# Kernel tuning notes

Measured on AMD Instinct MI355X. Metric: run time of the kernel, lower is better.

## Reference

```python
import jax, jax.numpy as jnp
import numpy as np

B, T, DIM, H = 32, 1024, 512, 8
HD = DIM // H
HID = int(DIM * 4.0)
EPS = 1e-6
SCALE = HD ** -0.5


def _ln(t, g, b):
    m = t.mean(-1, keepdims=True)
    var = ((t - m) ** 2).mean(-1, keepdims=True)
    return (t - m) * jax.lax.rsqrt(var + EPS) * g + b


def setup_inputs() -> dict:
    key = jax.random.key(0)
    ks = jax.random.split(key, 10)
    n = lambda k, s: jax.random.normal(k, s, dtype=jnp.float32)
    w = lambda k, s: n(k, s) * 0.02
    z = lambda d: jnp.zeros((d,), dtype=jnp.float32)
    o = lambda d: jnp.ones((d,), dtype=jnp.float32)
    return {
        'x': n(ks[0], (B, T, DIM)),
        'k': n(ks[1], (T, H, B, HD)),
        'v': n(ks[2], (T, H, B, HD)),
        'Wqkv': w(ks[3], (DIM, 3 * DIM)), 'bqkv': z(3 * DIM),
        'Wsa': w(ks[4], (DIM, DIM)), 'bsa': z(DIM),
        'Wq': w(ks[5], (DIM, DIM)), 'bq': z(DIM),
        'Wed': w(ks[6], (DIM, DIM)), 'bed': z(DIM),
        'g1': o(DIM), 'be1': z(DIM),
        'g2': o(DIM), 'be2': z(DIM),
        'g3': o(DIM), 'be3': z(DIM),
        'W1': w(ks[7], (DIM, HID)), 'b1': z(HID),
        'W2': w(ks[8], (HID, DIM)), 'b2': z(DIM),
    }


def _decoder_block(x, k, v, Wqkv, bqkv, Wsa, bsa, Wq, bq, Wed, bed,
                   g1, be1, g2, be2, g3, be3, W1, b1, W2, b2):
    # ---- self-attention (faithful to the original, degenerate einsums) ----
    qkv = x @ Wqkv + bqkv                                        # [B,T,3*DIM]
    qkv = qkv.reshape(B, T, 3, H, HD).transpose(2, 1, 3, 0, 4)   # [3,T,H,B,HD]
    q, sk, sv = qkv[0], qkv[1], qkv[2]
    dp = jnp.einsum('kabc,qdef->qabe', sk, q) * SCALE            # [T,H,B,B]
    scores = jax.nn.softmax(dp, axis=-1)
    wa = jnp.einsum('qabc,kdef->bqaf', scores, sv).reshape(B, T, DIM)
    attn = wa @ Wsa + bsa
    an1 = _ln(attn + x, g1, be1)
    # ---- encoder-decoder attention ----
    qe = (an1 @ Wq + bq).reshape(B, T, H, HD).transpose(1, 2, 0, 3)  # [T,H,B,HD]
    dp2 = jnp.einsum('abkd,abqd->abqk', k, qe) * SCALE           # [T,H,B,B]
    sc2 = jax.nn.softmax(dp2, axis=-1)
    wa2 = jnp.einsum('abts,abse->tabe', sc2, v).reshape(B, T, DIM)
    attn2 = wa2 @ Wed + bed
    an2 = _ln(attn2 + x, g2, be2)
    # ---- MLP (exact GELU, as nn.GELU default) ----
    hmid = jax.nn.gelu(an2 @ W1 + b1, approximate=False)
    z = hmid @ W2 + b2
    return _ln(z + an2, g3, be3)


def reference(x, k, v, Wqkv, bqkv, Wsa, bsa, Wq, bq, Wed, bed,
              g1, be1, g2, be2, g3, be3, W1, b1, W2, b2):
    return _decoder_block(x, k, v, Wqkv, bqkv, Wsa, bsa, Wq, bq, Wed, bed,
                          g1, be1, g2, be2, g3, be3, W1, b1, W2, b2)
```

## Files before the change

### kernel.cpp

```cpp
#include <hip/hip_runtime.h>
#include <hip/hip_bf16.h>
#include <math.h>

#define Bn 32
#define Tn 1024
#define DIMn 512
#define Hn 8
#define HDn 64
#define HIDn 2048
#define Mn 32768

using short8 = __attribute__((ext_vector_type(8))) short;
using half8  = __attribute__((ext_vector_type(8))) _Float16;
using f32x4  = __attribute__((ext_vector_type(4))) float;
typedef unsigned short u16;
typedef unsigned int   u32;

__device__ __forceinline__ u16 f2h(float x) {
  _Float16 h = (_Float16)x;
  return __builtin_bit_cast(u16, h);
}
__device__ __forceinline__ float h2f(u16 u) {
  return (float)__builtin_bit_cast(_Float16, u);
}
__device__ __forceinline__ u32 pack2h(float a, float b) {
  return (u32)f2h(a) | ((u32)f2h(b) << 16);
}
__device__ __forceinline__ void gld16(const void* g, void* l) {
  __builtin_amdgcn_global_load_lds((const __attribute__((address_space(1))) u32*)g,
                                   (__attribute__((address_space(3))) u32*)l, 16, 0, 0);
}
__device__ __forceinline__ float wredsum(float v) {
  #pragma unroll
  for (int d = 1; d < 64; d <<= 1) v += __shfl_xor(v, d, 64);
  return v;
}
__device__ __forceinline__ void hard_barrier() {
  asm volatile("" ::: "memory");
  __builtin_amdgcn_s_barrier();
  asm volatile("" ::: "memory");
}
__device__ __forceinline__ float fast_gelu(float v) {
  const float ax = fabsf(v) * 0.70710678118654752f;
  const float t = 1.0f / (1.0f + 0.3275911f * ax);
  const float p = ((((1.061405429f * t - 1.453152027f) * t) + 1.421413741f) * t - 0.284496736f) * t + 0.254829592f;
  const float y = 1.0f - p * t * __expf(-ax * ax);
  const float erfv = (v >= 0.f) ? y : -y;
  return 0.5f * v * (1.0f + erfv);
}

__global__ __launch_bounds__(256) void colsum1(const float* __restrict__ x, float* __restrict__ part) {
  const int b = blockIdx.x, t = threadIdx.x;
  const float* p = x + (size_t)b * 128 * DIMn;
  float a0 = 0.f, a1 = 0.f;
  for (int r = 0; r < 128; ++r) {
    a0 += p[r * DIMn + t];
    a1 += p[r * DIMn + t + 256];
  }
  part[b * DIMn + t] = a0;
  part[b * DIMn + t + 256] = a1;
}

__global__ __launch_bounds__(256) void colsum2(const float* __restrict__ part, float* __restrict__ xs) {
  const int c = blockIdx.x * 256 + threadIdx.x;
  float a = 0.f;
  for (int b = 0; b < 256; ++b) a += part[b * DIMn + c];
  xs[c] = a;
}

__global__ __launch_bounds__(256) void sv_k(const float* __restrict__ xs, const float* __restrict__ Wqkv,
                                            const float* __restrict__ bqkv, float* __restrict__ SVp) {
  __shared__ float xsh[512];
  __shared__ float red[4][64];
  const int h = blockIdx.x, q = threadIdx.x >> 6, f = threadIdx.x & 63;
  xsh[threadIdx.x] = xs[threadIdx.x];
  xsh[threadIdx.x + 256] = xs[threadIdx.x + 256];
  __syncthreads();
  const int colb = 2 * DIMn + h * HDn + f;
  float acc = 0.f;
  for (int i = q * 128; i < q * 128 + 128; ++i) acc += xsh[i] * Wqkv[(size_t)i * 1536 + colb];
  red[q][f] = acc;
  __syncthreads();
  if (q == 0)
    SVp[h * 64 + f] = red[0][f] + red[1][f] + red[2][f] + red[3][f] + 32768.0f * bqkv[colb];
}

__global__ __launch_bounds__(256) void attnc2_k(const float* __restrict__ SVp, const float* __restrict__ Wsa,
                                                const float* __restrict__ bsa, float* __restrict__ attnc) {
  __shared__ float SVs[64];
  __shared__ float red[4][64];
  const int q = threadIdx.x >> 6, jj = threadIdx.x & 63;
  if (threadIdx.x < 64) {
    float s = 0.f;
    #pragma unroll
    for (int h = 0; h < 8; ++h) s += SVp[h * 64 + threadIdx.x];
    SVs[threadIdx.x] = s;
  }
  __syncthreads();
  const int j = blockIdx.x * 64 + jj;
  float acc = 0.f;
  for (int i = q * 128; i < q * 128 + 128; ++i) acc += SVs[i & 63] * Wsa[(size_t)i * DIMn + j];
  red[q][jj] = acc;
  __syncthreads();
  if (q == 0) attnc[j] = red[0][jj] + red[1][jj] + red[2][jj] + red[3][jj] + bsa[j];
}

__global__ __launch_bounds__(256) void wtrans(const float* __restrict__ W, u16* __restrict__ WT, int K, int N) {
  __shared__ float tile[64][65];
  const int n0 = blockIdx.x * 64, k0 = blockIdx.y * 64;
  const int t = threadIdx.x;
  #pragma unroll
  for (int i = 0; i < 16; ++i) {
    const int fl = i * 256 + t, r = fl >> 6, c = fl & 63;
    tile[r][c] = W[(size_t)(k0 + r) * N + n0 + c];
  }
  __syncthreads();
  #pragma unroll
  for (int i = 0; i < 16; ++i) {
    const int fl = i * 256 + t, r = fl >> 6, c = fl & 63;
    WT[(size_t)(n0 + r) * K + k0 + c] = f2h(tile[c][r]);
  }
}

template <int MODE>
__global__ __launch_bounds__(256) void ln_k(const void* __restrict__ Ap, const void* __restrict__ Bp,
                                            const float* __restrict__ cv, const float* __restrict__ g,
                                            const float* __restrict__ be, void* __restrict__ outp) {
  const int row = blockIdx.x * 4 + (threadIdx.x >> 6);
  const int l = threadIdx.x & 63;
  const size_t base = (size_t)row * DIMn + l * 8;
  float v[8];
  if (MODE == 0 || MODE == 2) {
    const float* a = (const float*)Ap + base;
    float4 x0 = *(const float4*)a;
    float4 x1 = *(const float4*)(a + 4);
    v[0] = x0.x; v[1] = x0.y; v[2] = x0.z; v[3] = x0.w;
    v[4] = x1.x; v[5] = x1.y; v[6] = x1.z; v[7] = x1.w;
  } else {
    short8 s = *(const short8*)((const u16*)Ap + base);
    #pragma unroll
    for (int i = 0; i < 8; ++i) v[i] = h2f((u16)s[i]);
  }
  if (MODE == 0) {
    float4 c0 = *(const float4*)(cv + l * 8);
    float4 c1 = *(const float4*)(cv + l * 8 + 4);
    v[0] += c0.x; v[1] += c0.y; v[2] += c0.z; v[3] += c0.w;
    v[4] += c1.x; v[5] += c1.y; v[6] += c1.z; v[7] += c1.w;
  } else if (MODE == 1) {
    const float* b = (const float*)Bp + base;
    float4 x0 = *(const float4*)b;
    float4 x1 = *(const float4*)(b + 4);
    v[0] += x0.x; v[1] += x0.y; v[2] += x0.z; v[3] += x0.w;
    v[4] += x1.x; v[5] += x1.y; v[6] += x1.z; v[7] += x1.w;
  } else {
    short8 s2 = *(const short8*)((const u16*)Bp + base);
    #pragma unroll
    for (int i = 0; i < 8; ++i) v[i] += h2f((u16)s2[i]);
  }
  float s = 0.f;
  #pragma unroll
  for (int i = 0; i < 8; ++i) s += v[i];
  s = wredsum(s);
  const float mean = s * (1.0f / 512.0f);
  float q = 0.f;
  #pragma unroll
  for (int i = 0; i < 8; ++i) { const float d = v[i] - mean; q += d * d; }
  q = wredsum(q);
  const float rs = rsqrtf(q * (1.0f / 512.0f) + 1e-6f);
  float gg[8], bb[8];
  {
    float4 g0 = *(const float4*)(g + l * 8);
    float4 g1 = *(const float4*)(g + l * 8 + 4);
    float4 b0 = *(const float4*)(be + l * 8);
    float4 b1 = *(const float4*)(be + l * 8 + 4);
    gg[0] = g0.x; gg[1] = g0.y; gg[2] = g0.z; gg[3] = g0.w;
    gg[4] = g1.x; gg[5] = g1.y; gg[6] = g1.z; gg[7] = g1.w;
    bb[0] = b0.x; bb[1] = b0.y; bb[2] = b0.z; bb[3] = b0.w;
    bb[4] = b1.x; bb[5] = b1.y; bb[6] = b1.z; bb[7] = b1.w;
  }
  float y[8];
  #pragma unroll
  for (int i = 0; i < 8; ++i) y[i] = (v[i] - mean) * rs * gg[i] + bb[i];
  if (MODE == 2) {
    float* o = (float*)outp + base;
    *(float4*)o = make_float4(y[0], y[1], y[2], y[3]);
    *(float4*)(o + 4) = make_float4(y[4], y[5], y[6], y[7]);
  } else {
    short8 o;
    #pragma unroll
    for (int i = 0; i < 8; ++i) o[i] = (short)f2h(y[i]);
    *(short8*)((u16*)outp + base) = o;
  }
}

#define CPAD 132
template <bool GELU, bool OBF>
__global__ __launch_bounds__(256) void gemm_bt(const u16* __restrict__ A, const u16* __restrict__ BT,
                                               const float* __restrict__ bias, u16* __restrict__ OB,
                                               float* __restrict__ OF, int Ni, int Ki, int gridX) {
  __shared__ u16 smem[3 * 8192];
  const int tid = threadIdx.x;
  const int l = tid & 63, w = tid >> 6, wr = w >> 1, wc = w & 1;

  int wg = blockIdx.x;
  const int nwg = gridDim.x;
  if ((nwg & 7) == 0) {
    const int q = nwg >> 3;
    wg = (wg & 7) * q + (wg >> 3);
  }
  const int bx = wg % gridX, by = wg / gridX;
  const int m0 = by * 128, n0 = bx * 128;
  const int r16 = l & 15, g4 = l >> 4;

  const u16* ga = A + (size_t)(m0 + (tid >> 2)) * (size_t)Ki + (tid & 3) * 8;
  const u16* gb = BT + (size_t)(n0 + (tid >> 2)) * (size_t)Ki + (tid & 3) * 8;
  const int ldst = tid * 8;

  int aoff[4], boff[4];
  #pragma unroll
  for (int i = 0; i < 4; ++i) {
    aoff[i] = (wr * 64 + i * 16 + r16) * 32 + g4 * 8;
    boff[i] = 4096 + (wc * 64 + i * 16 + r16) * 32 + g4 * 8;
  }
  f32x4 acc[4][4] = {};

  const int nt = Ki >> 5;
  auto STAGE = [&](int t, int b) {
    u16* base = smem + b * 8192;
    const int kk = t * 32;
    gld16(ga + kk, &base[ldst]);
    gld16(ga + kk + (size_t)64 * Ki, &base[ldst + 2048]);
    gld16(gb + kk, &base[4096 + ldst]);
    gld16(gb + kk + (size_t)64 * Ki, &base[4096 + ldst + 2048]);
  };

  STAGE(0, 0);
  STAGE(1, 1);
  int b0 = 0, b1 = 1, b2 = 2;
  for (int t = 0; t < nt; ++t) {
    if (t < nt - 1) asm volatile("s_waitcnt vmcnt(4)" ::: "memory");
    else            asm volatile("s_waitcnt vmcnt(0)" ::: "memory");
    hard_barrier();
    if (t + 2 < nt) STAGE(t + 2, b2);
    const u16* base = smem + b0 * 8192;
    half8 af[4], bf[4];
    #pragma unroll
    for (int i = 0; i < 4; ++i) af[i] = *(const half8*)&base[aoff[i]];
    #pragma unroll
    for (int i = 0; i < 4; ++i) bf[i] = *(const half8*)&base[boff[i]];
    #pragma unroll
    for (int mi = 0; mi < 4; ++mi)
      #pragma unroll
      for (int ni = 0; ni < 4; ++ni)
        acc[mi][ni] = __builtin_amdgcn_mfma_f32_16x16x32_f16(af[mi], bf[ni], acc[mi][ni], 0, 0, 0);
    hard_barrier();
    const int tb = b0; b0 = b1; b1 = b2; b2 = tb;
  }

  if (OBF) {
    u16* Cs = smem;
    #pragma unroll
    for (int ni = 0; ni < 4; ++ni) {
      const int col = wc * 64 + ni * 16 + r16;
      const float bv = bias[n0 + col];
      #pragma unroll
      for (int mi = 0; mi < 4; ++mi) {
        const int rowb = wr * 64 + mi * 16 + g4 * 4;
        #pragma unroll
        for (int r = 0; r < 4; ++r) {
          float v = acc[mi][ni][r] + bv;
          if (GELU) v = fast_gelu(v);
          Cs[(rowb + r) * CPAD + col] = f2h(v);
        }
      }
    }
    hard_barrier();
    const int rr = tid >> 4;
    const int c0 = (tid & 15) * 8;
    #pragma unroll
    for (int j = 0; j < 8; ++j) {
      const int row = rr + j * 16;
      *(short8*)(OB + (size_t)(m0 + row) * Ni + n0 + c0) = *(const short8*)&Cs[row * CPAD + c0];
    }
  } else {
    #pragma unroll
    for (int ni = 0; ni < 4; ++ni) {
      const int col = n0 + wc * 64 + ni * 16 + r16;
      const float bv = bias[col];
      #pragma unroll
      for (int mi = 0; mi < 4; ++mi) {
        const int rowb = m0 + wr * 64 + mi * 16 + g4 * 4;
        #pragma unroll
        for (int r = 0; r < 4; ++r) {
          float v = acc[mi][ni][r] + bv;
          if (GELU) v = fast_gelu(v);
          OF[(size_t)(rowb + r) * Ni + col] = v;
        }
      }
    }
  }
}

__global__ __launch_bounds__(64) void attn_k(const u16* __restrict__ qe, const float* __restrict__ kin,
                                             const float* __restrict__ vin, u16* __restrict__ wa2) {
  const int t = blockIdx.x >> 3;
  const int h = blockIdx.x & 7;
  const int l = threadIdx.x;
  __shared__ u16 Kq[32 * 80];
  __shared__ u16 Qq[32 * 80];
  __shared__ u16 VT[64 * 48];
  __shared__ u16 Ps[32 * 48];

  const float* kp = kin + (size_t)blockIdx.x * 2048;
  const float* vp = vin + (size_t)blockIdx.x * 2048;
  #pragma unroll
  for (int i = 0; i < 8; ++i) {
    const int fl = i * 256 + l * 4;
    const int r = fl >> 6, c = fl & 63;
    float4 kv = *(const float4*)(kp + fl);
    float4 vv = *(const float4*)(vp + fl);
    *(u32*)&Kq[r * 80 + c]     = pack2h(kv.x, kv.y);
    *(u32*)&Kq[r * 80 + c + 2] = pack2h(kv.z, kv.w);
    VT[(c + 0) * 48 + r] = f2h(vv.x);
    VT[(c + 1) * 48 + r] = f2h(vv.y);
    VT[(c + 2) * 48 + r] = f2h(vv.z);
    VT[(c + 3) * 48 + r] = f2h(vv.w);
  }
  {
    const int qb = l >> 1, hf = l & 1;
    const u16* qp = qe + (size_t)(qb * Tn + t) * DIMn + h * HDn + hf * 32;
    #pragma unroll
    for (int j = 0; j < 4; ++j) {
      short8 d = *(const short8*)(qp + j * 8);
      *(short8*)&Qq[qb * 80 + hf * 32 + j * 8] = d;
    }
  }
  __syncthreads();

  const int r16 = l & 15, g4 = l >> 4;
  f32x4 sacc[2][2] = {};
  #pragma unroll
  for (int kk = 0; kk < 2; ++kk) {
    half8 aQ0 = *(const half8*)&Qq[r16 * 80 + kk * 32 + g4 * 8];
    half8 aQ1 = *(const half8*)&Qq[(16 + r16) * 80 + kk * 32 + g4 * 8];
    half8 bK0 = *(const half8*)&Kq[r16 * 80 + kk * 32 + g4 * 8];
    half8 bK1 = *(const half8*)&Kq[(16 + r16) * 80 + kk * 32 + g4 * 8];
    sacc[0][0] = __builtin_amdgcn_mfma_f32_16x16x32_f16(aQ0, bK0, sacc[0][0], 0, 0, 0);
    sacc[0][1] = __builtin_amdgcn_mfma_f32_16x16x32_f16(aQ0, bK1, sacc[0][1], 0, 0, 0);
    sacc[1][0] = __builtin_amdgcn_mfma_f32_16x16x32_f16(aQ1, bK0, sacc[1][0], 0, 0, 0);
    sacc[1][1] = __builtin_amdgcn_mfma_f32_16x16x32_f16(aQ1, bK1, sacc[1][1], 0, 0, 0);
  }
  #pragma unroll
  for (int m = 0; m < 2; ++m) {
    #pragma unroll
    for (int r = 0; r < 4; ++r) {
      const float a0 = sacc[m][0][r] * 0.125f;
      const float a1 = sacc[m][1][r] * 0.125f;
      float mx = fmaxf(a0, a1);
      #pragma unroll
      for (int d = 1; d < 16; d <<= 1) mx = fmaxf(mx, __shfl_xor(mx, d, 64));
      const float e0 = __expf(a0 - mx), e1 = __expf(a1 - mx);
      float sm = e0 + e1;
      #pragma unroll
      for (int d = 1; d < 16; d <<= 1) sm += __shfl_xor(sm, d, 64);
      const float inv = 1.0f / sm;
      const int rr = m * 16 + g4 * 4 + r;
      Ps[rr * 48 + r16]      = f2h(e0 * inv);
      Ps[rr * 48 + 16 + r16] = f2h(e1 * inv);
    }
  }
  __syncthreads();

  half8 aP0 = *(const half8*)&Ps[r16 * 48 + g4 * 8];
  half8 aP1 = *(const half8*)&Ps[(16 + r16) * 48 + g4 * 8];
  f32x4 oacc[2][4] = {};
  #pragma unroll
  for (int nn = 0; nn < 4; ++nn) {
    half8 bV = *(const half8*)&VT[(nn * 16 + r16) * 48 + g4 * 8];
    oacc[0][nn] = __builtin_amdgcn_mfma_f32_16x16x32_f16(aP0, bV, oacc[0][nn], 0, 0, 0);
    oacc[1][nn] = __builtin_amdgcn_mfma_f32_16x16x32_f16(aP1, bV, oacc[1][nn], 0, 0, 0);
  }
  #pragma unroll
  for (int m = 0; m < 2; ++m) {
    #pragma unroll
    for (int r = 0; r < 4; ++r) {
      const int qb = m * 16 + g4 * 4 + r;
      u16* op = wa2 + (size_t)(qb * Tn + t) * DIMn + h * HDn;
      #pragma unroll
      for (int nn = 0; nn < 4; ++nn)
        op[nn * 16 + r16] = f2h(oacc[m][nn][r]);
    }
  }
}

extern "C" void kernel_launch(void* const* d_in, const int* in_sizes, int n_in,
                              void* d_out, int out_size, void* d_ws, size_t ws_size,
                              hipStream_t stream) {
  (void)in_sizes; (void)n_in; (void)out_size;
  const float* x    = (const float*)d_in[0];
  const float* kin  = (const float*)d_in[1];
  const float* vin  = (const float*)d_in[2];
  const float* Wqkv = (const float*)d_in[3];
  const float* bqkv = (const float*)d_in[4];
  const float* Wsa  = (const float*)d_in[5];
  const float* bsa  = (const float*)d_in[6];
  const float* Wq   = (const float*)d_in[7];
  const float* bq   = (const float*)d_in[8];
  const float* Wed  = (const float*)d_in[9];
  const float* bed  = (const float*)d_in[10];
  const float* g1   = (const float*)d_in[11];
  const float* be1  = (const float*)d_in[12];
  const float* g2   = (const float*)d_in[13];
  const float* be2  = (const float*)d_in[14];
  const float* g3   = (const float*)d_in[15];
  const float* be3  = (const float*)d_in[16];
  const float* W1   = (const float*)d_in[17];
  const float* b1   = (const float*)d_in[18];
  const float* W2   = (const float*)d_in[19];
  const float* b2   = (const float*)d_in[20];

  char* ws = (char*)d_ws;
  float* xs    = (float*)(ws);
  float* SVp   = (float*)(ws + (2 << 10));
  float* attnc = (float*)(ws + (4 << 10));
  float* part  = (float*)(ws + (6 << 10));
  u16* wqT  = (u16*)(ws + (1 << 20));
  u16* wedT = (u16*)(ws + (1 << 20) + (512 << 10));
  u16* w1T  = (u16*)(ws + (2 << 20));
  u16* w2T  = (u16*)(ws + (4 << 20));
  u16* Abuf = (u16*)(ws + (6 << 20));
  const size_t HOFF = 38ull << 20;
  u16* hmid = (u16*)(ws + HOFF);

  u16* an1  = Abuf;
  u16* wa2  = Abuf;
  u16* an2b = Abuf;
  u16*   qe   = (u16*)d_out;
  u16*   a2bf = (u16*)d_out;
  float* zf   = (float*)d_out;

  long long avail = (long long)ws_size - (long long)HOFF;
  int crows = (avail > 0) ? (int)(avail / (HIDn * 2)) : 128;
  crows = (crows / 128) * 128;
  if (crows < 128) crows = 128;
  if (crows > Mn) crows = Mn;

  colsum1<<<256, 256, 0, stream>>>(x, part);
  colsum2<<<2, 256, 0, stream>>>(part, xs);
  sv_k<<<8, 256, 0, stream>>>(xs, Wqkv, bqkv, SVp);
  attnc2_k<<<8, 256, 0, stream>>>(SVp, Wsa, bsa, attnc);

  wtrans<<<dim3(8, 8),  256, 0, stream>>>(Wq,  wqT,  512, 512);
  wtrans<<<dim3(8, 8),  256, 0, stream>>>(Wed, wedT, 512, 512);
  wtrans<<<dim3(32, 8), 256, 0, stream>>>(W1,  w1T,  512, 2048);
  wtrans<<<dim3(8, 32), 256, 0, stream>>>(W2,  w2T,  2048, 512);

  ln_k<0><<<Mn / 4, 256, 0, stream>>>(x, nullptr, attnc, g1, be1, an1);
  gemm_bt<false, true><<<1024, 256, 0, stream>>>(an1, wqT, bq, qe, nullptr, 512, 512, 4);
  attn_k<<<Tn * Hn, 64, 0, stream>>>(qe, kin, vin, wa2);
  gemm_bt<false, true><<<1024, 256, 0, stream>>>(wa2, wedT, bed, a2bf, nullptr, 512, 512, 4);
  ln_k<1><<<Mn / 4, 256, 0, stream>>>(a2bf, x, nullptr, g2, be2, an2b);
  for (int r0 = 0; r0 < Mn; r0 += crows) {
    int rc = Mn - r0; if (rc > crows) rc = crows;
    gemm_bt<true, true><<<16 * (rc / 128), 256, 0, stream>>>(an2b + (size_t)r0 * DIMn, w1T, b1, hmid, nullptr, HIDn, DIMn, 16);
    gemm_bt<false, false><<<4 * (rc / 128), 256, 0, stream>>>(hmid, w2T, b2, nullptr, zf + (size_t)r0 * DIMn, DIMn, HIDn, 4);
  }
  ln_k<2><<<Mn / 4, 256, 0, stream>>>(zf, an2b, nullptr, g3, be3, d_out);
}
```

Baseline: 428.7 us.

## Enlarge GEMM tiles to 256x256 with 512-thread blocks

```diff
diff --git a/kernel.cpp b/kernel.cpp
--- a/kernel.cpp
+++ b/kernel.cpp
@@ -193,14 +193,14 @@
   }
 }
 
-#define CPAD 132
+#define CROW 272
 template <bool GELU, bool OBF>
-__global__ __launch_bounds__(256) void gemm_bt(const u16* __restrict__ A, const u16* __restrict__ BT,
+__global__ __launch_bounds__(512) void gemm_bt(const u16* __restrict__ A, const u16* __restrict__ BT,
                                                const float* __restrict__ bias, u16* __restrict__ OB,
                                                float* __restrict__ OF, int Ni, int Ki, int gridX) {
-  __shared__ u16 smem[3 * 8192];
+  __shared__ u16 smem[49152];
   const int tid = threadIdx.x;
-  const int l = tid & 63, w = tid >> 6, wr = w >> 1, wc = w & 1;
+  const int l = tid & 63, wid = tid >> 6, wr = wid >> 2, wc = wid & 3;
 
   int wg = blockIdx.x;
   const int nwg = gridDim.x;
@@ -209,29 +209,31 @@
     wg = (wg & 7) * q + (wg >> 3);
   }
   const int bx = wg % gridX, by = wg / gridX;
-  const int m0 = by * 128, n0 = bx * 128;
+  const int m0 = by * 256, n0 = bx * 256;
   const int r16 = l & 15, g4 = l >> 4;
 
-  const u16* ga = A + (size_t)(m0 + (tid >> 2)) * (size_t)Ki + (tid & 3) * 8;
-  const u16* gb = BT + (size_t)(n0 + (tid >> 2)) * (size_t)Ki + (tid & 3) * 8;
+  const int srow = tid >> 2, schunk = (tid & 3) * 8;
+  const u16* gaA = A  + (size_t)(m0 + srow) * (size_t)Ki + schunk;
+  const u16* gaB = BT + (size_t)(n0 + srow) * (size_t)Ki + schunk;
+  const size_t rowskip = (size_t)128 * (size_t)Ki;
   const int ldst = tid * 8;
 
-  int aoff[4], boff[4];
-  #pragma unroll
-  for (int i = 0; i < 4; ++i) {
-    aoff[i] = (wr * 64 + i * 16 + r16) * 32 + g4 * 8;
-    boff[i] = 4096 + (wc * 64 + i * 16 + r16) * 32 + g4 * 8;
-  }
-  f32x4 acc[4][4] = {};
-
+  int aoff[8], boff[4];
+  #pragma unroll
+  for (int mi = 0; mi < 8; ++mi) aoff[mi] = (wr * 128 + mi * 16 + r16) * 32 + g4 * 8;
+  #pragma unroll
+  for (int ni = 0; ni < 4; ++ni) boff[ni] = 8192 + (wc * 64 + ni * 16 + r16) * 32 + g4 * 8;
+
+  f32x4 acc[8][4] = {};
   const int nt = Ki >> 5;
+
   auto STAGE = [&](int t, int b) {
-    u16* base = smem + b * 8192;
+    u16* base = smem + b * 16384;
     const int kk = t * 32;
-    gld16(ga + kk, &base[ldst]);
-    gld16(ga + kk + (size_t)64 * Ki, &base[ldst + 2048]);
-    gld16(gb + kk, &base[4096 + ldst]);
-    gld16(gb + kk + (size_t)64 * Ki, &base[4096 + ldst + 2048]);
+    gld16(gaA + kk, &base[ldst]);
+    gld16(gaA + kk + rowskip, &base[ldst + 4096]);
+    gld16(gaB + kk, &base[8192 + ldst]);
+    gld16(gaB + kk + rowskip, &base[8192 + ldst + 4096]);
   };
 
   STAGE(0, 0);
@@ -242,57 +244,65 @@
     else            asm volatile("s_waitcnt vmcnt(0)" ::: "memory");
     hard_barrier();
     if (t + 2 < nt) STAGE(t + 2, b2);
-    const u16* base = smem + b0 * 8192;
-    half8 af[4], bf[4];
-    #pragma unroll
-    for (int i = 0; i < 4; ++i) af[i] = *(const half8*)&base[aoff[i]];
-    #pragma unroll
-    for (int i = 0; i < 4; ++i) bf[i] = *(const half8*)&base[boff[i]];
-    #pragma unroll
-    for (int mi = 0; mi < 4; ++mi)
+    const u16* base = smem + b0 * 16384;
+    half8 bf[4];
+    #pragma unroll
+    for (int ni = 0; ni < 4; ++ni) bf[ni] = *(const half8*)&base[boff[ni]];
+    #pragma unroll
+    for (int mi = 0; mi < 8; ++mi) {
+      half8 af = *(const half8*)&base[aoff[mi]];
       #pragma unroll
       for (int ni = 0; ni < 4; ++ni)
-        acc[mi][ni] = __builtin_amdgcn_mfma_f32_16x16x32_f16(af[mi], bf[ni], acc[mi][ni], 0, 0, 0);
+        acc[mi][ni] = __builtin_amdgcn_mfma_f32_16x16x32_f16(af, bf[ni], acc[mi][ni], 0, 0, 0);
+    }
     hard_barrier();
     const int tb = b0; b0 = b1; b1 = b2; b2 = tb;
   }
 
   if (OBF) {
     u16* Cs = smem;
+    float bv[4];
+    #pragma unroll
+    for (int ni = 0; ni < 4; ++ni) bv[ni] = bias[n0 + wc * 64 + ni * 16 + r16];
+    #pragma unroll
+    for (int p = 0; p < 2; ++p) {
+      #pragma unroll
+      for (int mi4 = 0; mi4 < 4; ++mi4) {
+        const int mi = p * 4 + mi4;
+        #pragma unroll
+        for (int ni = 0; ni < 4; ++ni) {
+          const int colL = wc * 64 + ni * 16 + r16;
+          #pragma unroll
+          for (int r = 0; r < 4; ++r) {
+            float v = acc[mi][ni][r] + bv[ni];
+            if (GELU) v = fast_gelu(v);
+            Cs[wr * (64 * CROW) + (mi4 * 16 + g4 * 4 + r) * CROW + colL] = f2h(v);
+          }
+        }
+      }
+      hard_barrier();
+      #pragma unroll
+      for (int j = 0; j < 8; ++j) {
+        const int s = tid + j * 512;
+        const int wrS = s >> 11;
+        const int rowL = (s & 2047) >> 5;
+        const int c8 = s & 31;
+        *(short8*)(OB + (size_t)(m0 + wrS * 128 + p * 64 + rowL) * Ni + n0 + c8 * 8) =
+            *(const short8*)&Cs[wrS * (64 * CROW) + rowL * CROW + c8 * 8];
+      }
+      if (p == 0) hard_barrier();
+    }
+  } else {
     #pragma unroll
     for (int ni = 0; ni < 4; ++ni) {
-      const int col = wc * 64 + ni * 16 + r16;
-      const float bv = bias[n0 + col];
-      #pragma unroll
-      for (int mi = 0; mi < 4; ++mi) {
-        const int rowb = wr * 64 + mi * 16 + g4 * 4;
+      const int col = n0 + wc * 64 + ni * 16 + r16;
+      const float bvv = bias[col];
+      #pragma unroll
+      for (int mi = 0; mi < 8; ++mi) {
+        const int rowb = m0 + wr * 128 + mi * 16 + g4 * 4;
         #pragma unroll
         for (int r = 0; r < 4; ++r) {
-          float v = acc[mi][ni][r] + bv;
-          if (GELU) v = fast_gelu(v);
-          Cs[(rowb + r) * CPAD + col] = f2h(v);
-        }
-      }
-    }
-    hard_barrier();
-    const int rr = tid >> 4;
-    const int c0 = (tid & 15) * 8;
-    #pragma unroll
-    for (int j = 0; j < 8; ++j) {
-      const int row = rr + j * 16;
-      *(short8*)(OB + (size_t)(m0 + row) * Ni + n0 + c0) = *(const short8*)&Cs[row * CPAD + c0];
-    }
-  } else {
-    #pragma unroll
-    for (int ni = 0; ni < 4; ++ni) {
-      const int col = n0 + wc * 64 + ni * 16 + r16;
-      const float bv = bias[col];
-      #pragma unroll
-      for (int mi = 0; mi < 4; ++mi) {
-        const int rowb = m0 + wr * 64 + mi * 16 + g4 * 4;
-        #pragma unroll
-        for (int r = 0; r < 4; ++r) {
-          float v = acc[mi][ni][r] + bv;
+          float v = acc[mi][ni][r] + bvv;
           if (GELU) v = fast_gelu(v);
           OF[(size_t)(rowb + r) * Ni + col] = v;
         }
@@ -440,9 +450,9 @@
   float* zf   = (float*)d_out;
 
   long long avail = (long long)ws_size - (long long)HOFF;
-  int crows = (avail > 0) ? (int)(avail / (HIDn * 2)) : 128;
-  crows = (crows / 128) * 128;
-  if (crows < 128) crows = 128;
+  int crows = (avail > 0) ? (int)(avail / (HIDn * 2)) : 256;
+  crows = (crows / 256) * 256;
+  if (crows < 256) crows = 256;
   if (crows > Mn) crows = Mn;
 
   colsum1<<<256, 256, 0, stream>>>(x, part);
@@ -456,14 +466,14 @@
   wtrans<<<dim3(8, 32), 256, 0, stream>>>(W2,  w2T,  2048, 512);
 
   ln_k<0><<<Mn / 4, 256, 0, stream>>>(x, nullptr, attnc, g1, be1, an1);
-  gemm_bt<false, true><<<1024, 256, 0, stream>>>(an1, wqT, bq, qe, nullptr, 512, 512, 4);
+  gemm_bt<false, true><<<256, 512, 0, stream>>>(an1, wqT, bq, qe, nullptr, 512, 512, 2);
   attn_k<<<Tn * Hn, 64, 0, stream>>>(qe, kin, vin, wa2);
-  gemm_bt<false, true><<<1024, 256, 0, stream>>>(wa2, wedT, bed, a2bf, nullptr, 512, 512, 4);
+  gemm_bt<false, true><<<256, 512, 0, stream>>>(wa2, wedT, bed, a2bf, nullptr, 512, 512, 2);
   ln_k<1><<<Mn / 4, 256, 0, stream>>>(a2bf, x, nullptr, g2, be2, an2b);
   for (int r0 = 0; r0 < Mn; r0 += crows) {
     int rc = Mn - r0; if (rc > crows) rc = crows;
-    gemm_bt<true, true><<<16 * (rc / 128), 256, 0, stream>>>(an2b + (size_t)r0 * DIMn, w1T, b1, hmid, nullptr, HIDn, DIMn, 16);
-    gemm_bt<false, false><<<4 * (rc / 128), 256, 0, stream>>>(hmid, w2T, b2, nullptr, zf + (size_t)r0 * DIMn, DIMn, HIDn, 4);
+    gemm_bt<true, true><<<8 * (rc / 256), 512, 0, stream>>>(an2b + (size_t)r0 * DIMn, w1T, b1, hmid, nullptr, HIDn, DIMn, 8);
+    gemm_bt<false, false><<<2 * (rc / 256), 512, 0, stream>>>(hmid, w2T, b2, nullptr, zf + (size_t)r0 * DIMn, DIMn, HIDn, 2);
   }
   ln_k<2><<<Mn / 4, 256, 0, stream>>>(zf, an2b, nullptr, g3, be3, d_out);
 }
```

Measured after the change: 414.7 us. 3.3% less time.
